# Kernel tuning notes

Hardware: AMD Instinct MI355X
Metric: run time of the kernel (lower is better)

The kernel has to match this reference:

```python
import jax, jax.numpy as jnp
import numpy as np

BLOCK_SIZE = 64


def setup_inputs() -> dict:
    key = jax.random.key(0)
    ks = jax.random.split(key, 10)
    n, c, d, h = 4, 1024, 768, 12          # batch, seq_len, hidden, heads
    E, M, P = 30, 4, 870                   # entities/doc, mentions/entity, pairs/doc
    emb, L = 768, 97                       # extractor emb, num relation labels
    return {
        "sequence_output": jax.random.normal(ks[0], (n, c, d), jnp.float32),
        "attention": jax.random.uniform(ks[1], (n, h, c, c), jnp.float32),
        "mention_idx": jax.random.randint(ks[2], (n, E, M), 0, c, jnp.int32),
        "mention_mask": jnp.ones((n, E, M), jnp.bool_),
        "hts": jax.random.randint(ks[3], (n, P, 2), 0, E, jnp.int32),
        "W_head": jax.random.normal(ks[4], (2 * d, emb), jnp.float32) * 0.02,
        "b_head": jnp.zeros((emb,), jnp.float32),
        "W_tail": jax.random.normal(ks[5], (2 * d, emb), jnp.float32) * 0.02,
        "b_tail": jnp.zeros((emb,), jnp.float32),
        "W_bil": jax.random.normal(ks[6], (emb * BLOCK_SIZE, L), jnp.float32) * 0.01,
        "b_bil": jnp.zeros((L,), jnp.float32),
    }


def reference(sequence_output, attention, mention_idx, mention_mask, hts,
              W_head, b_head, W_tail, b_tail, W_bil, b_bil):
    n, h, c, _ = attention.shape
    d = sequence_output.shape[-1]
    E, M = mention_idx.shape[1], mention_idx.shape[2]

    flat_idx = mention_idx.reshape(n, E * M)
    # gather mention token embeddings: [n, E, M, d]
    ment_emb = jnp.take_along_axis(sequence_output, flat_idx[:, :, None], axis=1)
    ment_emb = ment_emb.reshape(n, E, M, d)
    neg_inf = jnp.asarray(jnp.finfo(sequence_output.dtype).min, sequence_output.dtype)
    # logsumexp pooling over mentions (masked)
    e_emb = jax.scipy.special.logsumexp(
        jnp.where(mention_mask[..., None], ment_emb, neg_inf), axis=2)  # [n, E, d]

    # gather mention attention rows: attention[i, :, pos, :] -> [n, E, M, h, c]
    att_t = attention.transpose(0, 2, 1, 3)  # [n, c, h, c]
    ment_att = jnp.take_along_axis(att_t, flat_idx[:, :, None, None], axis=1)
    ment_att = ment_att.reshape(n, E, M, h, c)
    mcount = mention_mask.sum(axis=2).astype(attention.dtype)[:, :, None, None]
    e_att = (ment_att * mention_mask[..., None, None].astype(attention.dtype)).sum(axis=2)
    e_att = e_att / jnp.maximum(mcount, 1.0)  # [n, E, h, c]

    h_idx, t_idx = hts[..., 0], hts[..., 1]
    hs = jnp.take_along_axis(e_emb, h_idx[:, :, None], axis=1)            # [n, P, d]
    ts = jnp.take_along_axis(e_emb, t_idx[:, :, None], axis=1)
    h_att = jnp.take_along_axis(e_att, h_idx[:, :, None, None], axis=1)   # [n, P, h, c]
    t_att = jnp.take_along_axis(e_att, t_idx[:, :, None, None], axis=1)

    ht_att = (h_att * t_att).mean(axis=2)                                 # [n, P, c]
    ht_att = ht_att / (ht_att.sum(axis=-1, keepdims=True) + 1e-5)
    rs = jnp.einsum('nld,npl->npd', sequence_output, ht_att)              # [n, P, d]

    hs = hs.reshape(-1, d)
    ts = ts.reshape(-1, d)
    rs = rs.reshape(-1, d)
    hs = jnp.tanh(jnp.concatenate([hs, rs], axis=1) @ W_head + b_head)
    ts = jnp.tanh(jnp.concatenate([ts, rs], axis=1) @ W_tail + b_tail)

    emb = hs.shape[1]
    K = emb // BLOCK_SIZE
    b1 = hs.reshape(-1, K, BLOCK_SIZE)
    b2 = ts.reshape(-1, K, BLOCK_SIZE)
    # block outer products: [N, K, B, B] -> [N, emb*B]
    bl = (b1[:, :, :, None] * b2[:, :, None, :]).reshape(b1.shape[0], emb * BLOCK_SIZE)
    logits = bl @ W_bil + b_bil
    return logits
```

## Files before the change

kernel.cpp:

```cpp
#include <hip/hip_runtime.h>
#include <hip/hip_bf16.h>
#include <math.h>

#define N_B 4
#define C_  1024
#define D_  768
#define H_  12
#define E_  30
#define M_  4
#define P_  870
#define NP  (N_B*P_)
#define EMB 768
#define L_  97
#define LPAD 128
#define K2  (2*D_)

typedef __attribute__((ext_vector_type(8))) short s16x8;
typedef __attribute__((ext_vector_type(4))) short s16x4;
typedef __attribute__((ext_vector_type(4))) float fx4;

__device__ __forceinline__ float bfs2f(short s) {
  union { unsigned u; float f; } v; v.u = ((unsigned)(unsigned short)s) << 16; return v.f;
}
__device__ __forceinline__ short f2bfs(float f) {
  union { float f; unsigned u; } v; v.f = f;
  unsigned r = (v.u + 0x7FFFu + ((v.u >> 16) & 1u)) >> 16;
  return (short)(unsigned short)r;
}
__device__ __forceinline__ void pk2(short* dst, float a, float b) {
  __hip_bfloat162 p = __float22bfloat162_rn(make_float2(a, b));
  __builtin_memcpy(dst, &p, 4);
}
__device__ __forceinline__ void gll16(const void* g, void* l) {
  __builtin_amdgcn_global_load_lds(
      (__attribute__((address_space(1))) void*)(void*)g,
      (__attribute__((address_space(3))) void*)l, 16, 0, 0);
}

__device__ __forceinline__ void tcvt_body(const float* __restrict__ inb,
    short* __restrict__ outb, int R, int Cc, int r0, int c0,
    float* __restrict__ t , int tid) {
  int rr = tid >> 2, cq = (tid & 3) * 16;
#pragma unroll
  for (int q = 0; q < 16; ++q)
    t[rr*65 + cq + q] = inb[(size_t)(r0 + rr)*Cc + c0 + cq + q];
  __syncthreads();
  short tmp[16] __attribute__((aligned(16)));
#pragma unroll
  for (int q = 0; q < 16; ++q) tmp[q] = f2bfs(t[(cq + q)*65 + rr]);
  short* dst = outb + (size_t)(c0 + rr)*R + r0 + cq;
  *(s16x8*)dst = *(const s16x8*)&tmp[0];
  *(s16x8*)(dst + 8) = *(const s16x8*)&tmp[8];
}

__global__ __launch_bounds__(256) void k_prep(
    const float* __restrict__ seq, const float* __restrict__ att,
    const int* __restrict__ midx, const float* __restrict__ Wh,
    const float* __restrict__ Wt, const float* __restrict__ Wb,
    const float* __restrict__ bb,
    short* __restrict__ seqT, short* __restrict__ WhT, short* __restrict__ WtT,
    short* __restrict__ Wrb, short* __restrict__ e_emb,
    float* __restrict__ e_att, float* __restrict__ out) {
  __shared__ __align__(16) float smemf[64*98];
  int bid = blockIdx.x, tid = threadIdx.x;
  if (bid < 768) {
    int bz = bid / 192, r = bid % 192, bx = r & 15, by = r >> 4;
    tcvt_body(seq + (size_t)bz*C_*D_, seqT + (size_t)bz*D_*C_, C_, D_,
              bx*64, by*64, smemf, tid);
    return;
  }
  bid -= 768;
  if (bid < 576) {
    int bz = bid / 288, r = bid % 288, bx = r % 24, by = r / 24;
    tcvt_body(bz ? Wt : Wh, bz ? WtT : WhT, K2, EMB, bx*64, by*64, smemf, tid);
    return;
  }
  bid -= 576;
  if (bid < 768) {
    const float* src = Wb + (size_t)bid*64*L_;
    for (int c = tid; c < 64*L_; c += 256) {
      int j = c / L_, l = c - j*L_;
      smemf[j*98 + l] = src[c];
    }
    __syncthreads();
    short* dst = Wrb + (size_t)bid * (LPAD*64);
    for (int c = tid; c < LPAD*64; c += 256) {
      int l = c >> 6, js = c & 63;
      int jl = js ^ ((l & 7) << 3);
      dst[c] = (l < L_) ? f2bfs(smemf[jl*98 + l]) : (short)0;
    }
    return;
  }
  bid -= 768;
  if (bid < N_B*E_) {
    int b = bid / E_;
    int idx[M_];
#pragma unroll
    for (int m = 0; m < M_; ++m) idx[m] = midx[bid*M_ + m];
    if (tid < 192) {
      float v[M_][4];
#pragma unroll
      for (int m = 0; m < M_; ++m) {
        float4 x = *(const float4*)(seq + ((size_t)b*C_ + idx[m])*D_ + tid*4);
        v[m][0]=x.x; v[m][1]=x.y; v[m][2]=x.z; v[m][3]=x.w;
      }
      short tmp[4] __attribute__((aligned(8)));
#pragma unroll
      for (int c = 0; c < 4; ++c) {
        float mx = v[0][c];
#pragma unroll
        for (int m = 1; m < M_; ++m) mx = fmaxf(mx, v[m][c]);
        float s = 0.f;
#pragma unroll
        for (int m = 0; m < M_; ++m) s += expf(v[m][c] - mx);
        tmp[c] = f2bfs(mx + logf(s));
      }
      *(s16x4*)(e_emb + (size_t)bid*D_ + tid*4) = *(const s16x4*)tmp;
    }
    return;
  }
  bid -= N_B*E_;
  if (bid < N_B*E_*H_) {
    int head = bid % H_, be = bid / H_, b = be / E_;
    int idx[M_];
#pragma unroll
    for (int m = 0; m < M_; ++m) idx[m] = midx[be*M_ + m];
    const float* base = att + ((size_t)(b*H_ + head))*C_*C_;
    float4 a; a.x=0.f; a.y=0.f; a.z=0.f; a.w=0.f;
#pragma unroll
    for (int m = 0; m < M_; ++m) {
      float4 x = *(const float4*)(base + (size_t)idx[m]*C_ + tid*4);
      a.x += x.x; a.y += x.y; a.z += x.z; a.w += x.w;
    }
    const float inv = 1.f / (float)M_;
    a.x*=inv; a.y*=inv; a.z*=inv; a.w*=inv;
    *(float4*)(e_att + (size_t)bid*C_ + tid*4) = a;
    return;
  }
  bid -= N_B*E_*H_;
  {
    int i = bid*256 + tid;
    if (i < NP*L_) out[i] = bb[i % L_];
  }
}

__global__ __launch_bounds__(256) void k_htatt(const float* __restrict__ e_att,
    const int* __restrict__ hts, short* __restrict__ ht) {
  int bp = blockIdx.x;
  int b = bp / P_;
  int he = hts[bp*2 + 0], te = hts[bp*2 + 1];
  const float* ha = e_att + ((size_t)(b*E_ + he))*H_*C_;
  const float* ta = e_att + ((size_t)(b*E_ + te))*H_*C_;
  int t = threadIdx.x;
  float a0=0.f, a1=0.f, a2=0.f, a3=0.f;
#pragma unroll
  for (int hh = 0; hh < H_; ++hh) {
    float4 x = *(const float4*)(ha + (size_t)hh*C_ + t*4);
    float4 y = *(const float4*)(ta + (size_t)hh*C_ + t*4);
    a0 += x.x*y.x; a1 += x.y*y.y; a2 += x.z*y.z; a3 += x.w*y.w;
  }
  const float s = 1.f/12.f;
  a0*=s; a1*=s; a2*=s; a3*=s;
  float local = a0+a1+a2+a3;
#pragma unroll
  for (int off = 32; off > 0; off >>= 1) local += __shfl_down(local, off, 64);
  __shared__ float red[4];
  int wid = t >> 6, lane = t & 63;
  if (lane == 0) red[wid] = local;
  __syncthreads();
  float inv = 1.f / (red[0] + red[1] + red[2] + red[3] + 1e-5f);
  short tmp[4] __attribute__((aligned(8)));
  pk2(tmp,   a0*inv, a1*inv);
  pk2(tmp+2, a2*inv, a3*inv);
  *(s16x4*)(ht + (size_t)bp*C_ + t*4) = *(const s16x4*)tmp;
}

__global__ __launch_bounds__(256) void k_rs(const short* __restrict__ ht,
    const short* __restrict__ seqT, short* __restrict__ rsb) {
  int b = blockIdx.z;
  int p0 = blockIdx.y * 64;
  int n0 = blockIdx.x * 64;
  __shared__ __align__(16) short At[2][64][64];
  int tid = threadIdx.x, lane = tid & 63, w = tid >> 6;
  int r16 = lane & 15, quad = lane >> 4;
  int lr = lane >> 3;
  int colsw = ((lane & 7) ^ lr) * 8;
  int rA = p0 + w*16 + lr;      if (rA >= P_) rA = P_ - 1;
  int rB = p0 + w*16 + 8 + lr;  if (rB >= P_) rB = P_ - 1;
  const short* srcA = ht + ((size_t)(b*P_ + rA))*C_ + colsw;
  const short* srcB = ht + ((size_t)(b*P_ + rB))*C_ + colsw;
  const short* brow = seqT + ((size_t)(b*D_ + n0 + w*16 + r16))*C_ + quad*8;
  fx4 acc[4] = {};
  gll16(srcA, &At[0][w*16][0]);
  gll16(srcB, &At[0][w*16 + 8][0]);
  __syncthreads();
  int buf = 0;
  for (int k0 = 0; k0 < C_; k0 += 64) {
    s16x8 bf0 = *(const s16x8*)(brow + k0);
    s16x8 bf1 = *(const s16x8*)(brow + k0 + 32);
    if (k0 + 64 < C_) {
      gll16(srcA + k0 + 64, &At[buf^1][w*16][0]);
      gll16(srcB + k0 + 64, &At[buf^1][w*16 + 8][0]);
    }
#pragma unroll
    for (int mt = 0; mt < 4; ++mt) {
      int row = mt*16 + r16;
      const char* abase = (const char*)&At[buf][0][0] + row*128;
      s16x8 af0 = *(const s16x8*)(abase + ((quad*16)      ^ ((row & 7) << 4)));
      s16x8 af1 = *(const s16x8*)(abase + ((64 + quad*16) ^ ((row & 7) << 4)));
      acc[mt] = __builtin_amdgcn_mfma_f32_16x16x32_bf16(af0, bf0, acc[mt], 0, 0, 0);
      acc[mt] = __builtin_amdgcn_mfma_f32_16x16x32_bf16(af1, bf1, acc[mt], 0, 0, 0);
    }
    __syncthreads();
    buf ^= 1;
  }
#pragma unroll
  for (int mt = 0; mt < 4; ++mt)
#pragma unroll
    for (int reg = 0; reg < 4; ++reg) {
      int p = p0 + mt*16 + quad*4 + reg;
      if (p < P_) rsb[((size_t)(b*P_ + p))*D_ + n0 + w*16 + r16] = f2bfs(acc[mt][reg]);
    }
}

__global__ __launch_bounds__(256) void k_headtail(const short* __restrict__ e_emb,
    const short* __restrict__ rs, const int* __restrict__ hts,
    const short* __restrict__ WhT, const short* __restrict__ WtT,
    const float* __restrict__ bh, const float* __restrict__ bt,
    short* __restrict__ hsb, short* __restrict__ tsb) {
  int which = blockIdx.z;
  const short* WT = which ? WtT : WhT;
  const float* bias = which ? bt : bh;
  short* outp = which ? tsb : hsb;
  int pg0 = blockIdx.y * 64;
  int n0 = blockIdx.x * 128;
  __shared__ __align__(16) short At[2][64][64];
  int tid = threadIdx.x, lane = tid & 63, w = tid >> 6;
  int r16 = lane & 15, quad = lane >> 4;
  int lr = lane >> 3;
  int colsw = ((lane & 7) ^ lr) * 8;
  int pgA = pg0 + w*16 + lr;      if (pgA >= NP) pgA = 0;
  int pgB = pg0 + w*16 + 8 + lr;  if (pgB >= NP) pgB = 0;
  int bA = pgA / P_, bB = pgB / P_;
  int eA = hts[(size_t)pgA*2 + which], eB = hts[(size_t)pgB*2 + which];
  const short* embA = e_emb + ((size_t)(bA*E_ + eA))*D_ + colsw;
  const short* embB = e_emb + ((size_t)(bB*E_ + eB))*D_ + colsw;
  const short* rsA  = rs + (size_t)pgA*D_ + colsw;
  const short* rsB  = rs + (size_t)pgB*D_ + colsw;
  int nc0 = n0 + w*32;
  const short* bptr0 = WT + (size_t)(nc0 + r16)*K2 + quad*8;
  const short* bptr1 = WT + (size_t)(nc0 + 16 + r16)*K2 + quad*8;
  fx4 acc[4][2] = {};
  gll16(embA, &At[0][w*16][0]);
  gll16(embB, &At[0][w*16 + 8][0]);
  __syncthreads();
  int buf = 0;
  for (int k0 = 0; k0 < K2; k0 += 64) {
    s16x8 bfv[2][2];
#pragma unroll
    for (int ks = 0; ks < 2; ++ks) {
      bfv[ks][0] = *(const s16x8*)(bptr0 + k0 + ks*32);
      bfv[ks][1] = *(const s16x8*)(bptr1 + k0 + ks*32);
    }
    int kn = k0 + 64;
    if (kn < K2) {
      const short* sA = (kn < D_) ? (embA + kn) : (rsA + (kn - D_));
      const short* sB = (kn < D_) ? (embB + kn) : (rsB + (kn - D_));
      gll16(sA, &At[buf^1][w*16][0]);
      gll16(sB, &At[buf^1][w*16 + 8][0]);
    }
#pragma unroll
    for (int ks = 0; ks < 2; ++ks)
#pragma unroll
      for (int mt = 0; mt < 4; ++mt) {
        int row = mt*16 + r16;
        const char* abase = (const char*)&At[buf][0][0] + row*128;
        s16x8 af = *(const s16x8*)(abase + (((ks*64) + quad*16) ^ ((row & 7) << 4)));
        acc[mt][0] = __builtin_amdgcn_mfma_f32_16x16x32_bf16(af, bfv[ks][0], acc[mt][0], 0, 0, 0);
        acc[mt][1] = __builtin_amdgcn_mfma_f32_16x16x32_bf16(af, bfv[ks][1], acc[mt][1], 0, 0, 0);
      }
    __syncthreads();
    buf ^= 1;
  }
#pragma unroll
  for (int mt = 0; mt < 4; ++mt)
#pragma unroll
    for (int nt = 0; nt < 2; ++nt)
#pragma unroll
      for (int reg = 0; reg < 4; ++reg) {
        int pgw = pg0 + mt*16 + quad*4 + reg;
        if (pgw < NP) {
          int nn = nc0 + nt*16 + r16;
          outp[(size_t)pgw*EMB + nn] = f2bfs(tanhf(acc[mt][nt][reg] + bias[nn]));
        }
      }
}

__global__ __launch_bounds__(256, 3) void k_bilinear(const short* __restrict__ hsb,
    const short* __restrict__ tsb, const short* __restrict__ Wr,
    float* __restrict__ out) {
  int kx = blockIdx.x >> 1;
  int i0 = (blockIdx.x & 1) * 32;
  int p0 = blockIdx.y * 128;
  int tid = threadIdx.x, lane = tid & 63, w = tid >> 6;
  int r16 = lane & 15, quad = lane >> 4;

  __shared__ short HS[128][40];
  __shared__ __align__(16) short BT[2][LPAD][64];

  {
    int row = tid >> 1, half = (tid & 1) * 16;
    int pgr = p0 + row;
    s16x8 h0 = {0,0,0,0,0,0,0,0}, h1 = h0;
    if (pgr < NP) {
      const short* hp = hsb + (size_t)pgr*EMB + kx*64 + i0 + half;
      h0 = *(const s16x8*)hp; h1 = *(const s16x8*)(hp + 8);
    }
    *(s16x8*)&HS[row][half] = h0; *(s16x8*)&HS[row][half+8] = h1;
  }
  s16x8 tsv[2][2];
  int rowbase = p0 + w*32;
#pragma unroll
  for (int mt = 0; mt < 2; ++mt) {
    int pgr = rowbase + mt*16 + r16;
    if (pgr < NP) {
      const short* tp = tsb + (size_t)pgr*EMB + kx*64 + quad*8;
      tsv[mt][0] = *(const s16x8*)tp;
      tsv[mt][1] = *(const s16x8*)(tp + 32);
    } else {
      s16x8 z = {0,0,0,0,0,0,0,0};
      tsv[mt][0] = z; tsv[mt][1] = z;
    }
  }

  const short* wbase = Wr + (size_t)(kx*64 + i0)*(LPAD*64);
  {
#pragma unroll
    for (int u = 0; u < 4; ++u) {
      int chunk = u*4 + w;
      gll16(wbase + (size_t)chunk*512 + lane*8, (char*)&BT[0][0][0] + chunk*1024);
    }
  }
  __syncthreads();
  int buf = 0;
  fx4 acc[2][7] = {};
  for (int ii = 0; ii < 32; ++ii) {
    if (ii < 31) {
      const short* src = wbase + (size_t)(ii+1)*(LPAD*64);
#pragma unroll
      for (int u = 0; u < 4; ++u) {
        int chunk = u*4 + w;
        gll16(src + (size_t)chunk*512 + lane*8, (char*)&BT[buf^1][0][0] + chunk*1024);
      }
    }
    float hv0 = bfs2f(HS[w*32 + r16][ii]);
    float hv1 = bfs2f(HS[w*32 + 16 + r16][ii]);
#pragma unroll
    for (int ks = 0; ks < 2; ++ks) {
      s16x8 af0, af1;
#pragma unroll
      for (int e = 0; e < 8; e += 2) {
        short d2[2];
        pk2(d2, hv0*bfs2f(tsv[0][ks][e]), hv0*bfs2f(tsv[0][ks][e+1]));
        af0[e] = d2[0]; af0[e+1] = d2[1];
        pk2(d2, hv1*bfs2f(tsv[1][ks][e]), hv1*bfs2f(tsv[1][ks][e+1]));
        af1[e] = d2[0]; af1[e+1] = d2[1];
      }
#pragma unroll
      for (int nt = 0; nt < 7; ++nt) {
        int row = nt*16 + r16;
        const char* bbase = (const char*)&BT[buf][0][0] + row*128;
        s16x8 bf_ = *(const s16x8*)(bbase + (((ks*64) + quad*16) ^ ((row & 7) << 4)));
        acc[0][nt] = __builtin_amdgcn_mfma_f32_16x16x32_bf16(af0, bf_, acc[0][nt], 0, 0, 0);
        acc[1][nt] = __builtin_amdgcn_mfma_f32_16x16x32_bf16(af1, bf_, acc[1][nt], 0, 0, 0);
      }
    }
    __syncthreads();
    buf ^= 1;
  }
#pragma unroll
  for (int mt = 0; mt < 2; ++mt)
#pragma unroll
    for (int nt = 0; nt < 7; ++nt)
#pragma unroll
      for (int reg = 0; reg < 4; ++reg) {
        int pg = rowbase + mt*16 + quad*4 + reg;
        int l = nt*16 + r16;
        if (pg < NP && l < L_) atomicAdd(out + (size_t)pg*L_ + l, acc[mt][nt][reg]);
      }
}

extern "C" void kernel_launch(void* const* d_in, const int* in_sizes, int n_in,
                              void* d_out, int out_size, void* d_ws, size_t ws_size,
                              hipStream_t stream) {
  const float* seq   = (const float*)d_in[0];
  const float* att   = (const float*)d_in[1];
  const int*   midx  = (const int*)d_in[2];
  const int*   hts   = (const int*)d_in[4];
  const float* Wh    = (const float*)d_in[5];
  const float* bh    = (const float*)d_in[6];
  const float* Wt    = (const float*)d_in[7];
  const float* bt    = (const float*)d_in[8];
  const float* Wb    = (const float*)d_in[9];
  const float* bb    = (const float*)d_in[10];
  float* out = (float*)d_out;

  char* ws = (char*)d_ws;
  size_t off = 0;
  auto alloc = [&](size_t bytes) { void* p = ws + off; off = (off + bytes + 255) & ~(size_t)255; return p; };
  short* e_emb = (short*)alloc((size_t)N_B*E_*D_*2);
  float* e_att = (float*)alloc((size_t)N_B*E_*H_*C_*4);
  short* htb   = (short*)alloc((size_t)NP*C_*2);
  short* seqT  = (short*)alloc((size_t)N_B*D_*C_*2);
  short* rsb   = (short*)alloc((size_t)NP*D_*2);
  short* hsb   = (short*)alloc((size_t)NP*EMB*2);
  short* tsb   = (short*)alloc((size_t)NP*EMB*2);
  short* WhT   = (short*)alloc((size_t)EMB*K2*2);
  short* WtT   = (short*)alloc((size_t)EMB*K2*2);
  short* Wrb   = (short*)alloc((size_t)768*LPAD*64*2);
  (void)in_sizes; (void)n_in; (void)out_size; (void)ws_size;

  k_prep<<<dim3(4991), 256, 0, stream>>>(seq, att, midx, Wh, Wt, Wb, bb,
                                         seqT, WhT, WtT, Wrb, e_emb, e_att, out);
  k_htatt<<<NP, 256, 0, stream>>>(e_att, hts, htb);
  k_rs<<<dim3(D_/64, 14, N_B), 256, 0, stream>>>(htb, seqT, rsb);
  k_headtail<<<dim3(EMB/128, 55, 2), 256, 0, stream>>>(e_emb, rsb, hts, WhT, WtT, bh, bt, hsb, tsb);
  k_bilinear<<<dim3(24, 28), 256, 0, stream>>>(hsb, tsb, Wrb, out);
}
```

Before: 449.9 us.

## Replace bilinear atomics with partial buffers plus reduce; XCD-aware block remap; prefetch B

The bilinear kernel stops doing atomicAdd into the output and instead writes each K-chunk's partial tile to a padded workspace buffer. A new reduce kernel sums the 24 partials and adds the bias, so the bias-init step is removed from the prep kernel. The rs and bilinear grids are flattened and remapped so that neighbouring blocks on the same XCD share columns, aiming for better L2 locality. B-operand global loads in rs and headtail are software-prefetched one iteration ahead. This trades atomic contention for extra global memory traffic (about 38MB of partials) and one more launch.

```diff
diff --git a/kernel.cpp b/kernel.cpp
--- a/kernel.cpp
+++ b/kernel.cpp
@@ -10,8 +10,10 @@
 #define M_  4
 #define P_  870
 #define NP  (N_B*P_)
+#define NPPAD 3584
 #define EMB 768
 #define L_  97
+#define LP2 112
 #define LPAD 128
 #define K2  (2*D_)
 
@@ -57,10 +59,9 @@
     const float* __restrict__ seq, const float* __restrict__ att,
     const int* __restrict__ midx, const float* __restrict__ Wh,
     const float* __restrict__ Wt, const float* __restrict__ Wb,
-    const float* __restrict__ bb,
     short* __restrict__ seqT, short* __restrict__ WhT, short* __restrict__ WtT,
     short* __restrict__ Wrb, short* __restrict__ e_emb,
-    float* __restrict__ e_att, float* __restrict__ out) {
+    float* __restrict__ e_att) {
   __shared__ __align__(16) float smemf[64*98];
   int bid = blockIdx.x, tid = threadIdx.x;
   if (bid < 768) {
@@ -120,7 +121,7 @@
     return;
   }
   bid -= N_B*E_;
-  if (bid < N_B*E_*H_) {
+  {
     int head = bid % H_, be = bid / H_, b = be / E_;
     int idx[M_];
 #pragma unroll
@@ -135,12 +136,6 @@
     const float inv = 1.f / (float)M_;
     a.x*=inv; a.y*=inv; a.z*=inv; a.w*=inv;
     *(float4*)(e_att + (size_t)bid*C_ + tid*4) = a;
-    return;
-  }
-  bid -= N_B*E_*H_;
-  {
-    int i = bid*256 + tid;
-    if (i < NP*L_) out[i] = bb[i % L_];
   }
 }
 
@@ -177,9 +172,13 @@
 
 __global__ __launch_bounds__(256) void k_rs(const short* __restrict__ ht,
     const short* __restrict__ seqT, short* __restrict__ rsb) {
-  int b = blockIdx.z;
-  int p0 = blockIdx.y * 64;
-  int n0 = blockIdx.x * 64;
+  int id = blockIdx.x;
+  int xcd = id & 7, j = id >> 3;
+  int col = xcd + 8 * (j / 14);
+  int y = j % 14;
+  int b = col / 12;
+  int n0 = (col % 12) * 64;
+  int p0 = y * 64;
   __shared__ __align__(16) short At[2][64][64];
   int tid = threadIdx.x, lane = tid & 63, w = tid >> 6;
   int r16 = lane & 15, quad = lane >> 4;
@@ -193,12 +192,15 @@
   fx4 acc[4] = {};
   gll16(srcA, &At[0][w*16][0]);
   gll16(srcB, &At[0][w*16 + 8][0]);
+  s16x8 bc0 = *(const s16x8*)(brow);
+  s16x8 bc1 = *(const s16x8*)(brow + 32);
   __syncthreads();
   int buf = 0;
   for (int k0 = 0; k0 < C_; k0 += 64) {
-    s16x8 bf0 = *(const s16x8*)(brow + k0);
-    s16x8 bf1 = *(const s16x8*)(brow + k0 + 32);
+    s16x8 bn0 = bc0, bn1 = bc1;
     if (k0 + 64 < C_) {
+      bn0 = *(const s16x8*)(brow + k0 + 64);
+      bn1 = *(const s16x8*)(brow + k0 + 96);
       gll16(srcA + k0 + 64, &At[buf^1][w*16][0]);
       gll16(srcB + k0 + 64, &At[buf^1][w*16 + 8][0]);
     }
@@ -208,10 +210,11 @@
       const char* abase = (const char*)&At[buf][0][0] + row*128;
       s16x8 af0 = *(const s16x8*)(abase + ((quad*16)      ^ ((row & 7) << 4)));
       s16x8 af1 = *(const s16x8*)(abase + ((64 + quad*16) ^ ((row & 7) << 4)));
-      acc[mt] = __builtin_amdgcn_mfma_f32_16x16x32_bf16(af0, bf0, acc[mt], 0, 0, 0);
-      acc[mt] = __builtin_amdgcn_mfma_f32_16x16x32_bf16(af1, bf1, acc[mt], 0, 0, 0);
+      acc[mt] = __builtin_amdgcn_mfma_f32_16x16x32_bf16(af0, bc0, acc[mt], 0, 0, 0);
+      acc[mt] = __builtin_amdgcn_mfma_f32_16x16x32_bf16(af1, bc1, acc[mt], 0, 0, 0);
     }
     __syncthreads();
+    bc0 = bn0; bc1 = bn1;
     buf ^= 1;
   }
 #pragma unroll
@@ -253,17 +256,23 @@
   fx4 acc[4][2] = {};
   gll16(embA, &At[0][w*16][0]);
   gll16(embB, &At[0][w*16 + 8][0]);
+  s16x8 bc[2][2];
+#pragma unroll
+  for (int ks = 0; ks < 2; ++ks) {
+    bc[ks][0] = *(const s16x8*)(bptr0 + ks*32);
+    bc[ks][1] = *(const s16x8*)(bptr1 + ks*32);
+  }
   __syncthreads();
   int buf = 0;
   for (int k0 = 0; k0 < K2; k0 += 64) {
-    s16x8 bfv[2][2];
-#pragma unroll
-    for (int ks = 0; ks < 2; ++ks) {
-      bfv[ks][0] = *(const s16x8*)(bptr0 + k0 + ks*32);
-      bfv[ks][1] = *(const s16x8*)(bptr1 + k0 + ks*32);
-    }
     int kn = k0 + 64;
+    s16x8 bn[2][2] = {{bc[0][0], bc[0][1]}, {bc[1][0], bc[1][1]}};
     if (kn < K2) {
+#pragma unroll
+      for (int ks = 0; ks < 2; ++ks) {
+        bn[ks][0] = *(const s16x8*)(bptr0 + kn + ks*32);
+        bn[ks][1] = *(const s16x8*)(bptr1 + kn + ks*32);
+      }
       const short* sA = (kn < D_) ? (embA + kn) : (rsA + (kn - D_));
       const short* sB = (kn < D_) ? (embB + kn) : (rsB + (kn - D_));
       gll16(sA, &At[buf^1][w*16][0]);
@@ -276,10 +285,12 @@
         int row = mt*16 + r16;
         const char* abase = (const char*)&At[buf][0][0] + row*128;
         s16x8 af = *(const s16x8*)(abase + (((ks*64) + quad*16) ^ ((row & 7) << 4)));
-        acc[mt][0] = __builtin_amdgcn_mfma_f32_16x16x32_bf16(af, bfv[ks][0], acc[mt][0], 0, 0, 0);
-        acc[mt][1] = __builtin_amdgcn_mfma_f32_16x16x32_bf16(af, bfv[ks][1], acc[mt][1], 0, 0, 0);
+        acc[mt][0] = __builtin_amdgcn_mfma_f32_16x16x32_bf16(af, bc[ks][0], acc[mt][0], 0, 0, 0);
+        acc[mt][1] = __builtin_amdgcn_mfma_f32_16x16x32_bf16(af, bc[ks][1], acc[mt][1], 0, 0, 0);
       }
     __syncthreads();
+#pragma unroll
+    for (int ks = 0; ks < 2; ++ks) { bc[ks][0] = bn[ks][0]; bc[ks][1] = bn[ks][1]; }
     buf ^= 1;
   }
 #pragma unroll
@@ -298,10 +309,14 @@
 
 __global__ __launch_bounds__(256, 3) void k_bilinear(const short* __restrict__ hsb,
     const short* __restrict__ tsb, const short* __restrict__ Wr,
-    float* __restrict__ out) {
-  int kx = blockIdx.x >> 1;
-  int i0 = (blockIdx.x & 1) * 32;
-  int p0 = blockIdx.y * 128;
+    float* __restrict__ part) {
+  int id = blockIdx.x;
+  int xcd = id & 7, j = id >> 3;
+  int c = xcd + 8 * (j / 28);
+  int y = j % 28;
+  int kx = c >> 1;
+  int i0 = (c & 1) * 32;
+  int p0 = y * 128;
   int tid = threadIdx.x, lane = tid & 63, w = tid >> 6;
   int r16 = lane & 15, quad = lane >> 4;
 
@@ -378,16 +393,28 @@
     __syncthreads();
     buf ^= 1;
   }
+  float* pb = part + ((size_t)c * NPPAD + rowbase) * LP2;
 #pragma unroll
   for (int mt = 0; mt < 2; ++mt)
 #pragma unroll
     for (int nt = 0; nt < 7; ++nt)
 #pragma unroll
       for (int reg = 0; reg < 4; ++reg) {
-        int pg = rowbase + mt*16 + quad*4 + reg;
-        int l = nt*16 + r16;
-        if (pg < NP && l < L_) atomicAdd(out + (size_t)pg*L_ + l, acc[mt][nt][reg]);
-      }
+        int r = mt*16 + quad*4 + reg;
+        pb[(size_t)r*LP2 + nt*16 + r16] = acc[mt][nt][reg];
+      }
+}
+
+__global__ __launch_bounds__(256) void k_reduce(const float* __restrict__ part,
+    const float* __restrict__ bb, float* __restrict__ out) {
+  int i = blockIdx.x*256 + threadIdx.x;
+  if (i >= NP*L_) return;
+  int pg = i / L_, l = i - pg*L_;
+  float s = bb[l];
+#pragma unroll
+  for (int c = 0; c < 24; ++c)
+    s += part[((size_t)c * NPPAD + pg) * LP2 + l];
+  out[i] = s;
 }
 
 extern "C" void kernel_launch(void* const* d_in, const int* in_sizes, int n_in,
@@ -418,12 +445,14 @@
   short* WhT   = (short*)alloc((size_t)EMB*K2*2);
   short* WtT   = (short*)alloc((size_t)EMB*K2*2);
   short* Wrb   = (short*)alloc((size_t)768*LPAD*64*2);
+  float* part  = (float*)alloc((size_t)24*NPPAD*LP2*4);
   (void)in_sizes; (void)n_in; (void)out_size; (void)ws_size;
 
-  k_prep<<<dim3(4991), 256, 0, stream>>>(seq, att, midx, Wh, Wt, Wb, bb,
-                                         seqT, WhT, WtT, Wrb, e_emb, e_att, out);
+  k_prep<<<dim3(3672), 256, 0, stream>>>(seq, att, midx, Wh, Wt, Wb,
+                                         seqT, WhT, WtT, Wrb, e_emb, e_att);
   k_htatt<<<NP, 256, 0, stream>>>(e_att, hts, htb);
-  k_rs<<<dim3(D_/64, 14, N_B), 256, 0, stream>>>(htb, seqT, rsb);
+  k_rs<<<dim3(672), 256, 0, stream>>>(htb, seqT, rsb);
   k_headtail<<<dim3(EMB/128, 55, 2), 256, 0, stream>>>(e_emb, rsb, hts, WhT, WtT, bh, bt, hsb, tsb);
-  k_bilinear<<<dim3(24, 28), 256, 0, stream>>>(hsb, tsb, Wrb, out);
-}
+  k_bilinear<<<dim3(672), 256, 0, stream>>>(hsb, tsb, Wrb, part);
+  k_reduce<<<(NP*L_ + 255)/256, 256, 0, stream>>>(part, bb, out);
+}
```

After: 408.7 us. 1.1x faster.
